# Kernel tuning notes

Hardware: AMD Instinct MI355X
Metric: run time of the kernel (lower is better)

## Reference

```python
import jax, jax.numpy as jnp
import numpy as np

TAU = 5.0  # gumbel-softmax temperature from __init__ default tau=5.0


def setup_inputs() -> dict:
    key = jax.random.key(0)
    k0, k1, k2, k3 = jax.random.split(key, 4)
    B, N, C = 64, 576, 1024
    return {
        "vision_output": jax.random.normal(k0, (B, N, C), jnp.float32),
        "token_budget": jax.random.uniform(k1, (B,), jnp.float32),
        "budget_embedding": jax.random.normal(k2, (B, C), jnp.float32),
        "W": jax.random.normal(k3, (1, 2 * C), jnp.float32) * 0.02,  # logit_head weight [1, 2C]
        "b": jnp.zeros((1,), jnp.float32),  # logit_head bias
    }


def _iterative_topk_mask(logits, K, tau):
    """Vectorized n_times_gumbel_softmax (eval mode: no gumbel noise).
    Iteratively hard-selects the argmax of the (masked) softmax, with
    straight-through gradients, for K[b] steps per batch element.
    logits: [B, N], K: [B] int. Returns keep_mask [B, N] in {0,1} (forward).
    """
    B, N = logits.shape
    neg_inf = jnp.finfo(logits.dtype).min

    def step(mask, i):
        # mask forward values are exactly 0/1 (hard + soft - stop_grad(soft))
        masked = jnp.where(mask > 0, neg_inf, logits)
        soft = jax.nn.softmax(masked / tau, axis=-1)  # [B, N]
        hard = jax.nn.one_hot(jnp.argmax(soft, axis=-1), N, dtype=logits.dtype)
        y = hard + soft - jax.lax.stop_gradient(soft)  # straight-through
        active = (i < K).astype(logits.dtype)[:, None]  # per-sample variable K
        return mask + y * active, None

    mask, _ = jax.lax.scan(step, jnp.zeros_like(logits), jnp.arange(N))
    return mask


def reference(vision_output, token_budget, budget_embedding, W, b):
    B, N, C = vision_output.shape
    # K = clamp((ratio * N).long(), 1, N)  -- torch .long() truncates, as does astype
    K = jnp.clip((token_budget * N).astype(jnp.int32), 1, N)
    # concat each patch with its sample's budget embedding -> [B, N, 2C]
    pwb = jnp.concatenate(
        [vision_output, jnp.broadcast_to(budget_embedding[:, None, :], (B, N, C))],
        axis=-1,
    )
    logits = jnp.einsum("bnc,oc->bno", pwb, W)[..., 0] + b[0]  # [B, N]
    keep_mask = _iterative_topk_mask(logits, K, TAU)
    selected_features = vision_output * keep_mask[..., None]
    return selected_features, keep_mask
```

## Files before the change

kernel.cpp:

```cpp
#include <hip/hip_runtime.h>

#define B_ 64
#define N_ 576
#define C_ 1024
#define ROWS_PER_BLK 4

typedef float v4f __attribute__((ext_vector_type(4)));

__global__ __launch_bounds__(256) void k_logits(const float* __restrict__ V,
                                                const float* __restrict__ W,
                                                float* __restrict__ logits,
                                                int BN) {
    int wave = (int)((blockIdx.x * blockDim.x + threadIdx.x) >> 6);
    int lane = threadIdx.x & 63;
    if (wave >= BN) return;
    const v4f* v4 = (const v4f*)(V + (size_t)wave * C_);
    const v4f* w4 = (const v4f*)W;
    float acc = 0.f;
#pragma unroll
    for (int it = 0; it < C_ / (64 * 4); ++it) {
        v4f v = v4[lane + it * 64];
        v4f w = w4[lane + it * 64];
        acc += v.x * w.x + v.y * w.y + v.z * w.z + v.w * w.w;
    }
#pragma unroll
    for (int off = 32; off; off >>= 1) acc += __shfl_xor(acc, off, 64);
    if (lane == 0) logits[wave] = acc;
}

__global__ __launch_bounds__(N_) void k_mask(const float* __restrict__ logits,
                                             const float* __restrict__ token_budget,
                                             float* __restrict__ mask_out,
                                             float* __restrict__ mask_ws) {
    __shared__ float sl[N_];
    int b = blockIdx.x;
    int t = threadIdx.x;
    sl[t] = logits[b * N_ + t];
    __syncthreads();
    int K = (int)(token_budget[b] * (float)N_);
    K = K < 1 ? 1 : (K > N_ ? N_ : K);
    float ln = sl[t];
    int rank = 0;
#pragma unroll 8
    for (int m = 0; m < N_; ++m) {
        float lm = sl[m];
        rank += (lm > ln) || (lm == ln && m < t);
    }
    float mv = (rank < K) ? 1.0f : 0.0f;
    mask_out[b * N_ + t] = mv;
    mask_ws[b * N_ + t] = mv;
}

__global__ __launch_bounds__(256) void k_scale(const float* __restrict__ V,
                                               const float* __restrict__ mask,
                                               float* __restrict__ out) {
    int row0 = blockIdx.x * ROWS_PER_BLK;
    int t = threadIdx.x;
    const v4f z = {0.f, 0.f, 0.f, 0.f};
#pragma unroll
    for (int r = 0; r < ROWS_PER_BLK; ++r) {
        int row = row0 + r;
        float m = mask[row];
        const v4f* v4 = (const v4f*)(V + (size_t)row * C_);
        v4f* o4 = (v4f*)(out + (size_t)row * C_);
        if (m != 0.0f) {
            v4f v = v4[t];
            __builtin_nontemporal_store(v, &o4[t]);
        } else {
            __builtin_nontemporal_store(z, &o4[t]);
        }
    }
}

extern "C" void kernel_launch(void* const* d_in, const int* in_sizes, int n_in,
                              void* d_out, int out_size, void* d_ws, size_t ws_size,
                              hipStream_t stream) {
    const float* V  = (const float*)d_in[0];
    const float* tb = (const float*)d_in[1];
    const float* W  = (const float*)d_in[3];

    float* out_feat = (float*)d_out;
    float* out_mask = (float*)d_out + (size_t)B_ * N_ * C_;

    float* ws_logits = (float*)d_ws;
    float* ws_mask   = (float*)d_ws + B_ * N_;

    const int BN = B_ * N_;
    k_logits<<<(BN + 3) / 4, 256, 0, stream>>>(V, W, ws_logits, BN);
    k_mask<<<B_, N_, 0, stream>>>(ws_logits, tb, out_mask, ws_mask);
    k_scale<<<BN / ROWS_PER_BLK, 256, 0, stream>>>(V, ws_mask, out_feat);
}
```

Baseline: 283.0 us.

## Fuse rank-based mask computation into the scale kernel per row block

Merges the per-batch ranking kernel and the scale/copy kernel into one. Each 4-row block reloads its batch's 576 logits into shared memory, and each wave computes the rank of one row with a strided comparison plus a wave reduction. The block then uses that mask to copy or zero its rows. This removes one launch, the workspace round trip for the mask, and the poorly parallel 64-block ranking pass. In exchange every block redoes a small logits load and comparison loop.

```diff
diff --git a/kernel.cpp b/kernel.cpp
--- a/kernel.cpp
+++ b/kernel.cpp
@@ -28,41 +28,54 @@
     if (lane == 0) logits[wave] = acc;
 }
 
-__global__ __launch_bounds__(N_) void k_mask(const float* __restrict__ logits,
-                                             const float* __restrict__ token_budget,
-                                             float* __restrict__ mask_out,
-                                             float* __restrict__ mask_ws) {
+__global__ __launch_bounds__(256) void k_mask_scale(const float* __restrict__ V,
+                                                    const float* __restrict__ logits,
+                                                    const float* __restrict__ token_budget,
+                                                    float* __restrict__ out_feat,
+                                                    float* __restrict__ out_mask) {
     __shared__ float sl[N_];
-    int b = blockIdx.x;
+    __shared__ float smask[ROWS_PER_BLK];
+    int row0 = blockIdx.x * ROWS_PER_BLK;
+    int b = row0 / N_;
+    int n0 = row0 - b * N_;
     int t = threadIdx.x;
+
     sl[t] = logits[b * N_ + t];
+    sl[t + 256] = logits[b * N_ + t + 256];
+    if (t < 64) sl[t + 512] = logits[b * N_ + t + 512];
     __syncthreads();
+
     int K = (int)(token_budget[b] * (float)N_);
     K = K < 1 ? 1 : (K > N_ ? N_ : K);
-    float ln = sl[t];
-    int rank = 0;
-#pragma unroll 8
-    for (int m = 0; m < N_; ++m) {
-        float lm = sl[m];
-        rank += (lm > ln) || (lm == ln && m < t);
+
+    int w = t >> 6, l = t & 63;
+    {
+        int n = n0 + w;
+        float ln = sl[n];
+        int rank = 0;
+#pragma unroll
+        for (int i = 0; i < N_ / 64; ++i) {
+            int m = l + 64 * i;
+            float lm = sl[m];
+            rank += (lm > ln) || (lm == ln && m < n);
+        }
+#pragma unroll
+        for (int off = 32; off; off >>= 1) rank += __shfl_xor(rank, off, 64);
+        if (l == 0) {
+            float mv = (rank < K) ? 1.0f : 0.0f;
+            smask[w] = mv;
+            out_mask[b * N_ + n] = mv;
+        }
     }
-    float mv = (rank < K) ? 1.0f : 0.0f;
-    mask_out[b * N_ + t] = mv;
-    mask_ws[b * N_ + t] = mv;
-}
+    __syncthreads();
 
-__global__ __launch_bounds__(256) void k_scale(const float* __restrict__ V,
-                                               const float* __restrict__ mask,
-                                               float* __restrict__ out) {
-    int row0 = blockIdx.x * ROWS_PER_BLK;
-    int t = threadIdx.x;
     const v4f z = {0.f, 0.f, 0.f, 0.f};
 #pragma unroll
     for (int r = 0; r < ROWS_PER_BLK; ++r) {
         int row = row0 + r;
-        float m = mask[row];
+        float m = smask[r];
         const v4f* v4 = (const v4f*)(V + (size_t)row * C_);
-        v4f* o4 = (v4f*)(out + (size_t)row * C_);
+        v4f* o4 = (v4f*)(out_feat + (size_t)row * C_);
         if (m != 0.0f) {
             v4f v = v4[t];
             __builtin_nontemporal_store(v, &o4[t]);
@@ -83,10 +96,8 @@
     float* out_mask = (float*)d_out + (size_t)B_ * N_ * C_;
 
     float* ws_logits = (float*)d_ws;
-    float* ws_mask   = (float*)d_ws + B_ * N_;
 
     const int BN = B_ * N_;
     k_logits<<<(BN + 3) / 4, 256, 0, stream>>>(V, W, ws_logits, BN);
-    k_mask<<<B_, N_, 0, stream>>>(ws_logits, tb, out_mask, ws_mask);
-    k_scale<<<BN / ROWS_PER_BLK, 256, 0, stream>>>(V, ws_mask, out_feat);
+    k_mask_scale<<<BN / ROWS_PER_BLK, 256, 0, stream>>>(V, ws_logits, tb, out_feat, out_mask);
 }
```

After: 262.4 us (median of 2 runs). 7.3% less time.
